# Performance work log

Hardware: AMD Instinct MI355X
Metric: run time of the kernel (lower is better)

The kernel has to match this reference:

```python
import jax, jax.numpy as jnp
import numpy as np

HIDDEN = 768
MLP_HIDDEN = 3072
HEADS = 12
HEAD_DIM = HIDDEN // HEADS

def setup_inputs() -> dict:
    key = jax.random.key(0)
    ks = jax.random.split(key, 12)
    s = 0.02
    return {
        "x": jax.random.normal(ks[0], (16, 1024, HIDDEN), dtype=jnp.float32),
        "ln1_g": jnp.ones((HIDDEN,), jnp.float32),
        "ln1_b": jnp.zeros((HIDDEN,), jnp.float32),
        "wq": jax.random.normal(ks[1], (HIDDEN, HIDDEN), jnp.float32) * s,
        "wk": jax.random.normal(ks[2], (HIDDEN, HIDDEN), jnp.float32) * s,
        "wv": jax.random.normal(ks[3], (HIDDEN, HIDDEN), jnp.float32) * s,
        "wo": jax.random.normal(ks[4], (HIDDEN, HIDDEN), jnp.float32) * s,
        "bo": jnp.zeros((HIDDEN,), jnp.float32),
        "ln2_g": jnp.ones((HIDDEN,), jnp.float32),
        "ln2_b": jnp.zeros((HIDDEN,), jnp.float32),
        "w1": jax.random.normal(ks[5], (HIDDEN, MLP_HIDDEN), jnp.float32) * s,
        "b1": jnp.zeros((MLP_HIDDEN,), jnp.float32),
        "w2": jax.random.normal(ks[6], (MLP_HIDDEN, HIDDEN), jnp.float32) * s,
        "b2": jnp.zeros((HIDDEN,), jnp.float32),
    }

def _layernorm(x, g, b, eps=1e-5):
    mu = jnp.mean(x, axis=-1, keepdims=True)
    var = jnp.mean(jnp.square(x - mu), axis=-1, keepdims=True)
    return (x - mu) * jax.lax.rsqrt(var + eps) * g + b

def reference(x, ln1_g, ln1_b, wq, wk, wv, wo, bo, ln2_g, ln2_b, w1, b1, w2, b2):
    b, n, _ = x.shape
    h, d = HEADS, HEAD_DIM
    scale = d ** -0.5
    # Attention branch
    xn = _layernorm(x, ln1_g, ln1_b)
    q = (xn @ wq.T).reshape(b, n, h, d).transpose(0, 2, 1, 3)  # bhnd
    k = (xn @ wk.T).reshape(b, n, h, d).transpose(0, 2, 1, 3)
    v = (xn @ wv.T).reshape(b, n, h, d).transpose(0, 2, 1, 3)
    score = jax.nn.softmax(jnp.einsum('bhif,bhjf->bhij', q, k) * scale, axis=-1)
    attn = jnp.einsum('bhij,bhjf->bihf', score, v).reshape(b, n, h * d)
    x = attn @ wo.T + bo + x
    # MLP branch
    xn = _layernorm(x, ln2_g, ln2_b)
    hdn = jax.nn.gelu(xn @ w1 + b1, approximate=False)
    x = hdn @ w2 + b2 + x
    return x
```

## Files before the change

kernel.cpp:

```cpp
#include <hip/hip_runtime.h>
#include <hip/hip_bf16.h>

#define HIDDEN 768
#define MLPH   3072
#define HEADS  12
#define HD     64
#define SEQ    1024
#define BATCH  16
#define MTOT   (BATCH*SEQ)

typedef __attribute__((ext_vector_type(8))) short  short8;
typedef __attribute__((ext_vector_type(4))) short  short4x;
typedef __attribute__((ext_vector_type(8))) __bf16 bf16x8;
typedef __attribute__((ext_vector_type(4))) float  floatx4;

#define CL2 0.18033688011112042f

__device__ inline short f2bf(float f) {
  __hip_bfloat16 h = __float2bfloat16(f);
  return *reinterpret_cast<short*>(&h);
}

__device__ inline floatx4 mfma_bf16(short8 a, short8 b, floatx4 c) {
  return __builtin_amdgcn_mfma_f32_16x16x32_bf16(
      __builtin_bit_cast(bf16x8, a), __builtin_bit_cast(bf16x8, b), c, 0, 0, 0);
}

__device__ inline void gl_lds16(const short* g, short* l) {
  __builtin_amdgcn_global_load_lds(
      (const __attribute__((address_space(1))) unsigned int*)g,
      (__attribute__((address_space(3))) unsigned int*)l, 16, 0, 0);
}

__device__ inline float gelu_f(float x) {
  float z = 0.7978845608028654f * (x + 0.044715f * x * x * x);
  float e = __builtin_amdgcn_exp2f(z * 2.8853900817779268f);
  float t = 1.0f - 2.0f * __builtin_amdgcn_rcpf(e + 1.0f);
  return 0.5f * x * (1.0f + t);
}

__global__ __launch_bounds__(256) void conv_weights(
    const float* __restrict__ wq, const float* __restrict__ wk,
    const float* __restrict__ wv, const float* __restrict__ wo,
    const float* __restrict__ w1, const float* __restrict__ w2,
    short* __restrict__ wqkvb, short* __restrict__ wob,
    short* __restrict__ w1t,   short* __restrict__ w2t)
{
  int i = blockIdx.x * 256 + threadIdx.x;
  const int HH = HIDDEN * HIDDEN;
  if (i < HH) {
    wqkvb[i]        = f2bf(wq[i]);
    wqkvb[HH + i]   = f2bf(wk[i]);
    wqkvb[2*HH + i] = f2bf(wv[i]);
    wob[i]          = f2bf(wo[i]);
  }
  if (i < HIDDEN * MLPH) {
    int n = i / HIDDEN, k = i % HIDDEN;
    w1t[i] = f2bf(w1[(size_t)k * MLPH + n]);
    int n2 = i / MLPH, k2 = i % MLPH;
    w2t[i] = f2bf(w2[(size_t)k2 * HIDDEN + n2]);
  }
}

__global__ __launch_bounds__(256) void ln_kernel(
    const float* __restrict__ x, const float* __restrict__ g,
    const float* __restrict__ b, short* __restrict__ out)
{
  int row = blockIdx.x;
  const float* xr = x + (size_t)row * HIDDEN;
  int t = threadIdx.x;
  float v0 = xr[t], v1 = xr[t + 256], v2 = xr[t + 512];
  float s  = v0 + v1 + v2;
  float s2 = v0*v0 + v1*v1 + v2*v2;
  for (int off = 32; off > 0; off >>= 1) {
    s  += __shfl_down(s, off);
    s2 += __shfl_down(s2, off);
  }
  __shared__ float red[8];
  __shared__ float stats[2];
  int wave = t >> 6;
  if ((t & 63) == 0) { red[wave] = s; red[4 + wave] = s2; }
  __syncthreads();
  if (t == 0) {
    float S  = red[0] + red[1] + red[2] + red[3];
    float S2 = red[4] + red[5] + red[6] + red[7];
    float mu  = S * (1.0f / HIDDEN);
    float var = S2 * (1.0f / HIDDEN) - mu * mu;
    stats[0] = mu;
    stats[1] = rsqrtf(var + 1e-5f);
  }
  __syncthreads();
  float mu = stats[0], rs = stats[1];
  short* orow = out + (size_t)row * HIDDEN;
  orow[t]       = f2bf((v0 - mu) * rs * g[t]       + b[t]);
  orow[t + 256] = f2bf((v1 - mu) * rs * g[t + 256] + b[t + 256]);
  orow[t + 512] = f2bf((v2 - mu) * rs * g[t + 512] + b[t + 512]);
}

template<int OUTMODE , bool BIAS, bool GELU_E, bool RES,
         bool SCALEQ = false>
__global__ __launch_bounds__(512, 2) void gemm_bt2(
    const short* __restrict__ A, const short* __restrict__ B,
    const float* __restrict__ bias, const float* __restrict__ res,
    void* __restrict__ out, int M, int N, int K)
{
  __shared__ alignas(16) short As[2][2][8192];
  __shared__ alignas(16) short Bs[2][2][8192];

  int tid = threadIdx.x;
  int lane = tid & 63, wave = tid >> 6;
  int wr = wave >> 2, wc = wave & 3;
  int quad = lane >> 4, lc = lane & 15;

  int nbx = gridDim.x;
  int nwg = nbx * gridDim.y;
  int orig = blockIdx.y * nbx + blockIdx.x;
  int q8 = nwg >> 3, r8 = nwg & 7;
  int xcd = orig & 7, sub = orig >> 3;
  int wg = (xcd < r8 ? xcd * (q8 + 1) : r8 * (q8 + 1) + (xcd - r8) * q8) + sub;
  int m0 = (wg / nbx) * 256;
  int n0 = (wg % nbx) * 256;

  int srow = tid >> 2;
  int skb  = (tid & 3) ^ ((srow >> 1) & 3);
  const short* ga = A + (size_t)(m0 + srow) * K + skb * 8;
  const short* gb = B + (size_t)(n0 + srow) * K + skb * 8;
  const size_t rowskip = (size_t)128 * K;
  int lb0 = wave * 512;

#define STAGE_R(MAT, gp, sl, ks, kt) {                         \
    const short* _g = (gp) + (size_t)(kt) * 64 + (ks) * 32;    \
    gl_lds16(_g,           &MAT[sl][ks][lb0]);                 \
    gl_lds16(_g + rowskip, &MAT[sl][ks][4096 + lb0]);          \
  }

  floatx4 acc[8][4];
#pragma unroll
  for (int i = 0; i < 8; ++i)
#pragma unroll
    for (int j = 0; j < 4; ++j) acc[i][j] = floatx4{0.f, 0.f, 0.f, 0.f};

  int apos = (quad ^ ((lc >> 1) & 3)) * 8;
#define RD(buf, r) (*(const short8*)&(buf)[(r) * 32 + apos])

  int NK = K >> 6;

  STAGE_R(Bs, gb, 0, 1, 0); STAGE_R(Bs, gb, 0, 0, 0);
  STAGE_R(As, ga, 0, 0, 0); STAGE_R(As, ga, 0, 1, 0);

  for (int kt = 0; kt < NK; ++kt) {
    const int sl = kt & 1, s2 = sl ^ 1;
    const bool st = (kt + 1 < NK);
    const short* a0 = As[sl][0];
    const short* a1 = As[sl][1];
    const short* b0 = Bs[sl][0];
    const short* b1 = Bs[sl][1];
    short8 aF[8], bF[4];

    asm volatile("s_waitcnt vmcnt(2)" ::: "memory");
    __builtin_amdgcn_s_barrier();
    asm volatile("" ::: "memory");
    if (st) { STAGE_R(Bs, gb, s2, 1, kt + 1); STAGE_R(Bs, gb, s2, 0, kt + 1); }
#pragma unroll
    for (int j = 0; j < 4; ++j) bF[j] = RD(b0, wc * 64 + j * 16 + lc);
#pragma unroll
    for (int i = 0; i < 8; ++i) aF[i] = RD(a0, wr * 128 + i * 16 + lc);
#pragma unroll
    for (int i = 0; i < 8; ++i)
#pragma unroll
      for (int j = 0; j < 4; ++j)
        acc[i][j] = mfma_bf16(aF[i], bF[j], acc[i][j]);

    if (st) asm volatile("s_waitcnt vmcnt(4)" ::: "memory");
    else    asm volatile("s_waitcnt vmcnt(0)" ::: "memory");
    __builtin_amdgcn_s_barrier();
    asm volatile("" ::: "memory");
    if (st) { STAGE_R(As, ga, s2, 0, kt + 1); STAGE_R(As, ga, s2, 1, kt + 1); }
#pragma unroll
    for (int j = 0; j < 4; ++j) bF[j] = RD(b1, wc * 64 + j * 16 + lc);
#pragma unroll
    for (int i = 0; i < 8; ++i) aF[i] = RD(a1, wr * 128 + i * 16 + lc);
#pragma unroll
    for (int i = 0; i < 8; ++i)
#pragma unroll
      for (int j = 0; j < 4; ++j)
        acc[i][j] = mfma_bf16(aF[i], bF[j], acc[i][j]);
  }
#undef STAGE_R
#undef RD

#pragma unroll
  for (int i = 0; i < 8; ++i)
#pragma unroll
    for (int j = 0; j < 4; ++j)
#pragma unroll
      for (int r = 0; r < 4; ++r) {
        int row = m0 + wr * 128 + i * 16 + quad * 4 + r;
        int col = n0 + wc * 64 + j * 16 + lc;
        float v = acc[i][j][r];
        if (BIAS)   v += bias[col];
        if (GELU_E) v = gelu_f(v);
        if (RES)    v += res[(size_t)row * N + col];
        if (SCALEQ && col < HIDDEN) v *= CL2;
        if (OUTMODE == 1) ((short*)out)[(size_t)row * N + col] = f2bf(v);
        else              ((float*)out)[(size_t)row * N + col] = v;
      }
}

__global__ __launch_bounds__(256) void vtrans_kernel(
    const short* __restrict__ qkv, short* __restrict__ vtg)
{
  int kt = blockIdx.x, h = blockIdx.y, b = blockIdx.z;
  int t = threadIdx.x;
  __shared__ short Vl[64][72];
  const short* vb = qkv + (size_t)(b * SEQ + kt * 64) * 2304 + 1536 + h * 64;
  int row = t >> 2, seg = t & 3;
  short8 r0 = *(const short8*)(vb + (size_t)row * 2304 + seg * 16);
  short8 r1 = *(const short8*)(vb + (size_t)row * 2304 + seg * 16 + 8);
  *(short8*)&Vl[row][seg * 16]     = r0;
  *(short8*)&Vl[row][seg * 16 + 8] = r1;
  __syncthreads();
  int ks = t >> 7, d = (t & 127) >> 1, hb = t & 1;
  short8 w0;
#pragma unroll
  for (int u = 0; u < 8; ++u) {
    int blk = hb * 2 + (u >> 3), j = u & 7;
    int ksrc = ks * 32 + (blk ^ ((d >> 1) & 3)) * 8 + j;
    w0[u] = Vl[ksrc][d];
  }
  short8 w1;
#pragma unroll
  for (int u = 8; u < 16; ++u) {
    int blk = hb * 2 + (u >> 3), j = u & 7;
    int ksrc = ks * 32 + (blk ^ ((d >> 1) & 3)) * 8 + j;
    w1[u - 8] = Vl[ksrc][d];
  }
  short* o = vtg + ((size_t)((b * HEADS + h) * 16 + kt)) * 4096 + t * 16;
  *(short8*)o       = w0;
  *(short8*)(o + 8) = w1;
}

__global__ __launch_bounds__(512) void attn_kernel(
    const short* __restrict__ qkv, const short* __restrict__ vtg,
    short* __restrict__ out)
{
  int qt = blockIdx.x;
  int h  = blockIdx.y;
  int b  = blockIdx.z;
  int tid = threadIdx.x, lane = tid & 63, wave = tid >> 6;
  int quad = lane >> 4, lc = lane & 15;

  __shared__ alignas(16) short Qs[2 * 128 * 32];
  __shared__ alignas(16) short Ks[2 * 64 * 32];
  __shared__ alignas(16) short Vs[2 * 64 * 32];
  __shared__ alignas(16) short Ps[8][16 * 72];

  const int LDQ = 3 * HIDDEN;
  const short* qb = qkv + (size_t)(b * SEQ) * LDQ + h * HD;
  const short* kb = qb + HIDDEN;
  const short* vt = vtg + (size_t)((b * HEADS + h) * 16) * 4096;

  {
    int row = tid >> 2, blk = tid & 3;
    int kblk = blk ^ ((row >> 1) & 3);
#pragma unroll
    for (int t = 0; t < 2; ++t) {
      const short* g = qb + (size_t)(qt * 128 + row) * LDQ + t * 32 + kblk * 8;
      gl_lds16(g, &Qs[t * 4096 + wave * 512]);
    }
  }
  __syncthreads();

  int pos = quad ^ ((lc >> 1) & 3);
  short8 aq[2];
#pragma unroll
  for (int ks = 0; ks < 2; ++ks)
    aq[ks] = *(const short8*)&Qs[ks * 4096 + (wave * 16 + lc) * 32 + pos * 8];

  floatx4 oacc[4];
#pragma unroll
  for (int n2 = 0; n2 < 4; ++n2) oacc[n2] = floatx4{0.f, 0.f, 0.f, 0.f};
  float lsum = 0.f;

  int srow = (tid >> 2) & 63;
  int sks  = tid >> 8;
  int skb  = (tid & 3) ^ ((srow >> 1) & 3);
  const short* kg0 = kb + (size_t)srow * LDQ + sks * 32 + skb * 8;
  const short* vg0 = vt + tid * 8;
  short* pw = &Ps[wave][0];

  for (int kt = 0; kt < 16; ++kt) {
    gl_lds16(kg0 + (size_t)(kt * 64) * LDQ, &Ks[wave * 512]);
    gl_lds16(vg0 + kt * 4096, &Vs[wave * 512]);
    __syncthreads();

    floatx4 sacc[4];
#pragma unroll
    for (int m2 = 0; m2 < 4; ++m2) sacc[m2] = floatx4{0.f, 0.f, 0.f, 0.f};
#pragma unroll
    for (int ks = 0; ks < 2; ++ks) {
#pragma unroll
      for (int m2 = 0; m2 < 4; ++m2) {
        short8 ak = *(const short8*)&Ks[ks * 2048 + (m2 * 16 + lc) * 32 + pos * 8];
        sacc[m2] = mfma_bf16(ak, aq[ks], sacc[m2]);
      }
    }

#pragma unroll
    for (int m2 = 0; m2 < 4; ++m2) {
      float p0 = exp2f(sacc[m2][0]);
      float p1 = exp2f(sacc[m2][1]);
      float p2 = exp2f(sacc[m2][2]);
      float p3 = exp2f(sacc[m2][3]);
      lsum += (p0 + p1) + (p2 + p3);
      short4x pk;
      pk[0] = f2bf(p0); pk[1] = f2bf(p1); pk[2] = f2bf(p2); pk[3] = f2bf(p3);
      *(short4x*)&pw[lc * 72 + m2 * 16 + quad * 4] = pk;
    }
    asm volatile("s_waitcnt lgkmcnt(0)" ::: "memory");
    __builtin_amdgcn_sched_barrier(0);

#pragma unroll
    for (int ks = 0; ks < 2; ++ks) {
      short8 ap = *(const short8*)&pw[lc * 72 + (ks * 4 + quad) * 8];
#pragma unroll
      for (int n2 = 0; n2 < 4; ++n2) {
        short8 bv = *(const short8*)&Vs[ks * 2048 + (n2 * 16 + lc) * 32 + pos * 8];
        oacc[n2] = mfma_bf16(ap, bv, oacc[n2]);
      }
    }
    __syncthreads();
  }

  float rs = lsum;
  rs += __shfl_xor(rs, 16);
  rs += __shfl_xor(rs, 32);
#pragma unroll
  for (int r = 0; r < 4; ++r) {
    float inv = 1.0f / __shfl(rs, quad * 4 + r);
    int row = b * SEQ + qt * 128 + wave * 16 + quad * 4 + r;
#pragma unroll
    for (int n2 = 0; n2 < 4; ++n2) {
      int col = h * HD + n2 * 16 + lc;
      out[(size_t)row * HIDDEN + col] = f2bf(oacc[n2][r] * inv);
    }
  }
}

extern "C" void kernel_launch(void* const* d_in, const int* in_sizes, int n_in,
                              void* d_out, int out_size, void* d_ws, size_t ws_size,
                              hipStream_t stream) {
  const float* x    = (const float*)d_in[0];
  const float* ln1g = (const float*)d_in[1];
  const float* ln1b = (const float*)d_in[2];
  const float* wq   = (const float*)d_in[3];
  const float* wk   = (const float*)d_in[4];
  const float* wv   = (const float*)d_in[5];
  const float* wo   = (const float*)d_in[6];
  const float* bo   = (const float*)d_in[7];
  const float* ln2g = (const float*)d_in[8];
  const float* ln2b = (const float*)d_in[9];
  const float* w1   = (const float*)d_in[10];
  const float* b1   = (const float*)d_in[11];
  const float* w2   = (const float*)d_in[12];
  const float* b2   = (const float*)d_in[13];

  auto rup = [](size_t b) { return (b + 255) & ~(size_t)255; };
  const size_t wbytes = rup((size_t)3 * HIDDEN * HIDDEN * 2) +
                        rup((size_t)HIDDEN * HIDDEN * 2) +
                        rup((size_t)MLPH * HIDDEN * 2) +
                        rup((size_t)HIDDEN * MLPH * 2);

  int R = SEQ;
  const int cands[4] = {16384, 8192, 4096, 2048};
  for (int i = 0; i < 4; ++i) {
    size_t need = wbytes + rup((size_t)cands[i] * 1536) + rup((size_t)cands[i] * 6144)
                         + rup((size_t)cands[i] * 1536);
    if (need <= ws_size) { R = cands[i]; break; }
  }

  char* ws = (char*)d_ws;
  size_t off = 0;
  auto alloc = [&](size_t bytes) {
    char* p = ws + off;
    off += (bytes + 255) & ~(size_t)255;
    return p;
  };
  short* wqkvb = (short*)alloc((size_t)3 * HIDDEN * HIDDEN * 2);
  short* wob   = (short*)alloc((size_t)HIDDEN * HIDDEN * 2);
  short* w1t   = (short*)alloc((size_t)MLPH * HIDDEN * 2);
  short* w2t   = (short*)alloc((size_t)HIDDEN * MLPH * 2);
  short* slotA = (short*)alloc((size_t)R * 1536);
  short* bigR  = (short*)alloc((size_t)R * 6144);
  short* vtg   = (short*)alloc((size_t)R * 1536);

  conv_weights<<<(HIDDEN * MLPH + 255) / 256, 256, 0, stream>>>(
      wq, wk, wv, wo, w1, w2, wqkvb, wob, w1t, w2t);

  const int nch = MTOT / R;
  for (int c = 0; c < nch; ++c) {
    const float* xc  = x + (size_t)c * R * HIDDEN;
    float*       x2c = (float*)d_out + (size_t)c * R * HIDDEN;

    ln_kernel<<<R, 256, 0, stream>>>(xc, ln1g, ln1b, slotA);
    gemm_bt2<1, false, false, false, true>
        <<<dim3((3 * HIDDEN) / 256, R / 256), 512, 0, stream>>>(
        slotA, wqkvb, nullptr, nullptr, bigR, R, 3 * HIDDEN, HIDDEN);
    vtrans_kernel<<<dim3(16, HEADS, R / SEQ), 256, 0, stream>>>(bigR, vtg);
    attn_kernel<<<dim3(SEQ / 128, HEADS, R / SEQ), 512, 0, stream>>>(
        bigR, vtg, slotA);
    gemm_bt2<0, true, false, true>
        <<<dim3(HIDDEN / 256, R / 256), 512, 0, stream>>>(
        slotA, wob, bo, xc, x2c, R, HIDDEN, HIDDEN);
    ln_kernel<<<R, 256, 0, stream>>>(x2c, ln2g, ln2b, slotA);
    gemm_bt2<1, true, true, false>
        <<<dim3(MLPH / 256, R / 256), 512, 0, stream>>>(
        slotA, w1t, b1, nullptr, bigR, R, MLPH, HIDDEN);
    gemm_bt2<0, true, false, true>
        <<<dim3(HIDDEN / 256, R / 256), 512, 0, stream>>>(
        bigR, w2t, b2, x2c, x2c, R, HIDDEN, MLPH);
  }
}
```

Baseline: 673.5 us.

## Shrink GEMM tile to 128x256 with BK=32 and single-barrier pipeline

The GEMM block tile is reduced from 256x256 to 128x256, with a K step of 32 instead of 64. LDS use drops from 64KB to 24KB per block and per-thread accumulators halve, so launch bounds now request 4 blocks per CU. The K loop becomes one-stage prefetch with a single wait per iteration, an explicit lgkmcnt wait, a sched_barrier and raised priority around the MFMA block. This buys occupancy and more blocks per grid at the cost of less data reuse per tile and more barriers per unit of work.

```diff
diff --git a/kernel.cpp b/kernel.cpp
--- a/kernel.cpp
+++ b/kernel.cpp
@@ -99,13 +99,13 @@
 
 template<int OUTMODE , bool BIAS, bool GELU_E, bool RES,
          bool SCALEQ = false>
-__global__ __launch_bounds__(512, 2) void gemm_bt2(
+__global__ __launch_bounds__(512, 4) void gemm_bt2(
     const short* __restrict__ A, const short* __restrict__ B,
     const float* __restrict__ bias, const float* __restrict__ res,
     void* __restrict__ out, int M, int N, int K)
 {
-  __shared__ alignas(16) short As[2][2][8192];
-  __shared__ alignas(16) short Bs[2][2][8192];
+  __shared__ alignas(16) short As[2][4096];
+  __shared__ alignas(16) short Bs[2][8192];
 
   int tid = threadIdx.x;
   int lane = tid & 63, wave = tid >> 6;
@@ -118,7 +118,7 @@
   int q8 = nwg >> 3, r8 = nwg & 7;
   int xcd = orig & 7, sub = orig >> 3;
   int wg = (xcd < r8 ? xcd * (q8 + 1) : r8 * (q8 + 1) + (xcd - r8) * q8) + sub;
-  int m0 = (wg / nbx) * 256;
+  int m0 = (wg / nbx) * 128;
   int n0 = (wg % nbx) * 256;
 
   int srow = tid >> 2;
@@ -128,74 +128,65 @@
   const size_t rowskip = (size_t)128 * K;
   int lb0 = wave * 512;
 
-#define STAGE_R(MAT, gp, sl, ks, kt) {                         \
-    const short* _g = (gp) + (size_t)(kt) * 64 + (ks) * 32;    \
-    gl_lds16(_g,           &MAT[sl][ks][lb0]);                 \
-    gl_lds16(_g + rowskip, &MAT[sl][ks][4096 + lb0]);          \
-  }
-
-  floatx4 acc[8][4];
-#pragma unroll
-  for (int i = 0; i < 8; ++i)
+#define STAGE(SL, KT) {                                        \
+    const size_t _ko = (size_t)(KT) * 32;                      \
+    gl_lds16(ga + _ko,           &As[SL][lb0]);                \
+    gl_lds16(gb + _ko,           &Bs[SL][lb0]);                \
+    gl_lds16(gb + _ko + rowskip, &Bs[SL][4096 + lb0]);         \
+  }
+
+  floatx4 acc[4][4];
+#pragma unroll
+  for (int i = 0; i < 4; ++i)
 #pragma unroll
     for (int j = 0; j < 4; ++j) acc[i][j] = floatx4{0.f, 0.f, 0.f, 0.f};
 
   int apos = (quad ^ ((lc >> 1) & 3)) * 8;
-#define RD(buf, r) (*(const short8*)&(buf)[(r) * 32 + apos])
-
-  int NK = K >> 6;
-
-  STAGE_R(Bs, gb, 0, 1, 0); STAGE_R(Bs, gb, 0, 0, 0);
-  STAGE_R(As, ga, 0, 0, 0); STAGE_R(As, ga, 0, 1, 0);
+
+  int NK = K >> 5;
+
+  STAGE(0, 0);
 
   for (int kt = 0; kt < NK; ++kt) {
-    const int sl = kt & 1, s2 = sl ^ 1;
+    const int sl = kt & 1;
     const bool st = (kt + 1 < NK);
-    const short* a0 = As[sl][0];
-    const short* a1 = As[sl][1];
-    const short* b0 = Bs[sl][0];
-    const short* b1 = Bs[sl][1];
-    short8 aF[8], bF[4];
-
-    asm volatile("s_waitcnt vmcnt(2)" ::: "memory");
+    if (st) {
+      STAGE(sl ^ 1, kt + 1);
+      asm volatile("s_waitcnt vmcnt(3)" ::: "memory");
+    } else {
+      asm volatile("s_waitcnt vmcnt(0)" ::: "memory");
+    }
     __builtin_amdgcn_s_barrier();
     asm volatile("" ::: "memory");
-    if (st) { STAGE_R(Bs, gb, s2, 1, kt + 1); STAGE_R(Bs, gb, s2, 0, kt + 1); }
-#pragma unroll
-    for (int j = 0; j < 4; ++j) bF[j] = RD(b0, wc * 64 + j * 16 + lc);
-#pragma unroll
-    for (int i = 0; i < 8; ++i) aF[i] = RD(a0, wr * 128 + i * 16 + lc);
-#pragma unroll
-    for (int i = 0; i < 8; ++i)
+
+    short8 aF[4], bF[4];
+#pragma unroll
+    for (int i = 0; i < 4; ++i)
+      aF[i] = *(const short8*)&As[sl][(wr * 64 + i * 16 + lc) * 32 + apos];
+#pragma unroll
+    for (int j = 0; j < 4; ++j)
+      bF[j] = *(const short8*)&Bs[sl][(wc * 64 + j * 16 + lc) * 32 + apos];
+    asm volatile("s_waitcnt lgkmcnt(0)" ::: "memory");
+    __builtin_amdgcn_sched_barrier(0);
+    __builtin_amdgcn_s_setprio(1);
+#pragma unroll
+    for (int i = 0; i < 4; ++i)
 #pragma unroll
       for (int j = 0; j < 4; ++j)
         acc[i][j] = mfma_bf16(aF[i], bF[j], acc[i][j]);
-
-    if (st) asm volatile("s_waitcnt vmcnt(4)" ::: "memory");
-    else    asm volatile("s_waitcnt vmcnt(0)" ::: "memory");
+    __builtin_amdgcn_s_setprio(0);
     __builtin_amdgcn_s_barrier();
     asm volatile("" ::: "memory");
-    if (st) { STAGE_R(As, ga, s2, 0, kt + 1); STAGE_R(As, ga, s2, 1, kt + 1); }
-#pragma unroll
-    for (int j = 0; j < 4; ++j) bF[j] = RD(b1, wc * 64 + j * 16 + lc);
-#pragma unroll
-    for (int i = 0; i < 8; ++i) aF[i] = RD(a1, wr * 128 + i * 16 + lc);
-#pragma unroll
-    for (int i = 0; i < 8; ++i)
-#pragma unroll
-      for (int j = 0; j < 4; ++j)
-        acc[i][j] = mfma_bf16(aF[i], bF[j], acc[i][j]);
-  }
-#undef STAGE_R
-#undef RD
-
-#pragma unroll
-  for (int i = 0; i < 8; ++i)
+  }
+#undef STAGE
+
+#pragma unroll
+  for (int i = 0; i < 4; ++i)
 #pragma unroll
     for (int j = 0; j < 4; ++j)
 #pragma unroll
       for (int r = 0; r < 4; ++r) {
-        int row = m0 + wr * 128 + i * 16 + quad * 4 + r;
+        int row = m0 + wr * 64 + i * 16 + quad * 4 + r;
         int col = n0 + wc * 64 + j * 16 + lc;
         float v = acc[i][j][r];
         if (BIAS)   v += bias[col];
@@ -404,20 +395,20 @@
 
     ln_kernel<<<R, 256, 0, stream>>>(xc, ln1g, ln1b, slotA);
     gemm_bt2<1, false, false, false, true>
-        <<<dim3((3 * HIDDEN) / 256, R / 256), 512, 0, stream>>>(
+        <<<dim3((3 * HIDDEN) / 256, R / 128), 512, 0, stream>>>(
         slotA, wqkvb, nullptr, nullptr, bigR, R, 3 * HIDDEN, HIDDEN);
     vtrans_kernel<<<dim3(16, HEADS, R / SEQ), 256, 0, stream>>>(bigR, vtg);
     attn_kernel<<<dim3(SEQ / 128, HEADS, R / SEQ), 512, 0, stream>>>(
         bigR, vtg, slotA);
     gemm_bt2<0, true, false, true>
-        <<<dim3(HIDDEN / 256, R / 256), 512, 0, stream>>>(
+        <<<dim3(HIDDEN / 256, R / 128), 512, 0, stream>>>(
         slotA, wob, bo, xc, x2c, R, HIDDEN, HIDDEN);
     ln_kernel<<<R, 256, 0, stream>>>(x2c, ln2g, ln2b, slotA);
     gemm_bt2<1, true, true, false>
-        <<<dim3(MLPH / 256, R / 256), 512, 0, stream>>>(
+        <<<dim3(MLPH / 256, R / 128), 512, 0, stream>>>(
         slotA, w1t, b1, nullptr, bigR, R, MLPH, HIDDEN);
     gemm_bt2<0, true, false, true>
-        <<<dim3(HIDDEN / 256, R / 256), 512, 0, stream>>>(
+        <<<dim3(HIDDEN / 256, R / 128), 512, 0, stream>>>(
         bigR, w2t, b2, x2c, x2c, R, HIDDEN, MLPH);
   }
 }
```

Measured after the change: 579.2 us. 14.0% less time.
